# Kernel optimization log

Hardware: AMD Instinct MI355X
Metric: run time of the kernel (lower is better)

The kernel has to match this reference:

```python
import jax, jax.numpy as jnp
import numpy as np
import math
from jax import lax

B, T, C = 32, 512, 256
NL, NH, FF = 2, 4, 1024
DH = C // NH
NFREQ = 64   # n_even//2 for d_model=256 (even dims interleave sin/cos)
N_ODD = 128  # odd dims carry learned ramp a*t+b
MIN_P, MAX_P = 4.0, 10000.0


def setup_inputs() -> dict:
    key = jax.random.key(0)
    ks = jax.random.split(key, 16)
    def nrm(k, shape, s=0.02):
        return (jax.random.normal(k, shape) * s).astype(jnp.float32)
    x = jax.random.normal(ks[0], (B, T, C), jnp.float32)
    # strictly increasing normalized timestamps
    dts = jax.random.uniform(ks[1], (B, T), jnp.float32) * 0.02 + 1e-3
    ts = jnp.cumsum(dts, axis=1)
    return {
        "x": x, "ts": ts,
        "gru_Wih": nrm(ks[2], (3 * C, C)), "gru_Whh": nrm(ks[3], (3 * C, C)),
        "gru_bih": jnp.zeros((3 * C,), jnp.float32), "gru_bhh": jnp.zeros((3 * C,), jnp.float32),
        "ode_W": nrm(ks[4], (C, 4 * C)), "ode_b": jnp.zeros((C,), jnp.float32),
        "norm_ode_g": jnp.ones((C,), jnp.float32), "norm_ode_b": jnp.zeros((C,), jnp.float32),
        "norm_gru_g": jnp.ones((C,), jnp.float32), "norm_gru_b": jnp.zeros((C,), jnp.float32),
        "film_W": nrm(ks[5], (2 * C, C)), "film_b": jnp.zeros((2 * C,), jnp.float32),
        "te_a": nrm(ks[6], (N_ODD,), 1.0), "te_b": nrm(ks[7], (N_ODD,), 0.1),
        "qkv_W": nrm(ks[8], (NL, 3 * C, C)), "qkv_b": jnp.zeros((NL, 3 * C), jnp.float32),
        "out_W": nrm(ks[9], (NL, C, C)), "out_b": jnp.zeros((NL, C), jnp.float32),
        "ln1_g": jnp.ones((NL, C), jnp.float32), "ln1_b": jnp.zeros((NL, C), jnp.float32),
        "ln2_g": jnp.ones((NL, C), jnp.float32), "ln2_b": jnp.zeros((NL, C), jnp.float32),
        "ff1_W": nrm(ks[10], (NL, FF, C)), "ff1_b": jnp.zeros((NL, FF), jnp.float32),
        "ff2_W": nrm(ks[11], (NL, C, FF)), "ff2_b": jnp.zeros((NL, C), jnp.float32),
        "lnf_g": jnp.ones((C,), jnp.float32), "lnf_b": jnp.zeros((C,), jnp.float32),
    }


def _ln(x, g, b, eps=1e-5):
    m = x.mean(-1, keepdims=True)
    v = ((x - m) ** 2).mean(-1, keepdims=True)
    return (x - m) / jnp.sqrt(v + eps) * g + b


def _forward(x, ts, gru_Wih, gru_Whh, gru_bih, gru_bhh, ode_W, ode_b,
             norm_ode_g, norm_ode_b, norm_gru_g, norm_gru_b, film_W, film_b,
             te_a, te_b, qkv_W, qkv_b, out_W, out_b, ln1_g, ln1_b, ln2_g, ln2_b,
             ff1_W, ff1_b, ff2_W, ff2_b, lnf_g, lnf_b):
    Bx, Tx, Cx = x.shape

    def gru(xi, h):  # PyTorch GRUCell math
        gi = xi @ gru_Wih.T + gru_bih
        gh = h @ gru_Whh.T + gru_bhh
        ir, iz, inn = jnp.split(gi, 3, -1)
        hr, hz, hn = jnp.split(gh, 3, -1)
        r = jax.nn.sigmoid(ir + hr)
        z = jax.nn.sigmoid(iz + hz)
        n = jnp.tanh(inn + r * hn)
        return (1.0 - z) * n + z * h

    def step(h, inp):  # RK4 ODE jump + GRU jump per event
        xi, xp, dt = inp  # (B,C),(B,C),(B,1)
        dx = (xi - xp) / dt
        def f(hh):
            return jnp.tanh(jnp.concatenate([hh, xi, xp, dx], -1) @ ode_W.T + ode_b)
        k1 = f(h)
        k2 = f(h + 0.5 * dt * k1)
        k3 = f(h + 0.5 * dt * k2)
        k4 = f(h + dt * k3)
        h = h + dt / 6.0 * (k1 + 2.0 * k2 + 2.0 * k3 + k4)
        h = _ln(h, norm_ode_g, norm_ode_b)
        h = _ln(gru(xi, h), norm_gru_g, norm_gru_b)
        return h, h

    h0 = _ln(gru(x[:, 0], jnp.zeros((Bx, Cx), x.dtype)), norm_gru_g, norm_gru_b)
    xs = (x[:, 1:].swapaxes(0, 1), x[:, :-1].swapaxes(0, 1),
          (ts[:, 1:] - ts[:, :-1])[..., None].swapaxes(0, 1))
    _, ys = lax.scan(step, h0, xs)
    h = jnp.concatenate([h0[None], ys], 0).swapaxes(0, 1)  # (B,T,C)

    # FiLM params from hidden states
    gb = jax.nn.silu(h) @ film_W.T + film_b
    gamma, beta = jnp.split(gb, 2, -1)

    # TimeHybridEncoding: even dims interleaved sin/cos, odd dims learned ramp
    freqs = jnp.exp(-jnp.linspace(0.0, math.log(MAX_P / MIN_P), NFREQ)) * (2.0 * math.pi / MIN_P)
    phase = ts[..., None] * freqs  # (B,T,NFREQ)
    sc = jnp.stack([jnp.sin(phase), jnp.cos(phase)], -1).reshape(Bx, Tx, 2 * NFREQ)
    ramp = ts[..., None] * te_a + te_b  # (B,T,N_ODD)
    tme = jnp.zeros((Bx, Tx, Cx), x.dtype)
    tme = tme.at[..., 0::2].set(sc).at[..., 1::2].set(ramp)
    tme = (1.0 + gamma) * tme + beta

    # Pre-LN TransformerEncoder (eval mode: dropout off), relu FFN, final LN
    H = h + tme
    scale = 1.0 / jnp.sqrt(jnp.float32(DH))
    for l in range(NL):
        a = _ln(H, ln1_g[l], ln1_b[l])
        qkv = a @ qkv_W[l].T + qkv_b[l]
        q, k, v = jnp.split(qkv, 3, -1)
        q = q.reshape(Bx, Tx, NH, DH).transpose(0, 2, 1, 3)
        k = k.reshape(Bx, Tx, NH, DH).transpose(0, 2, 1, 3)
        v = v.reshape(Bx, Tx, NH, DH).transpose(0, 2, 1, 3)
        att = jax.nn.softmax(jnp.einsum('bhqd,bhkd->bhqk', q, k) * scale, axis=-1)
        o = jnp.einsum('bhqk,bhkd->bhqd', att, v).transpose(0, 2, 1, 3).reshape(Bx, Tx, Cx)
        H = H + o @ out_W[l].T + out_b[l]
        f2 = _ln(H, ln2_g[l], ln2_b[l])
        H = H + jax.nn.relu(f2 @ ff1_W[l].T + ff1_b[l]) @ ff2_W[l].T + ff2_b[l]
    return _ln(H, lnf_g, lnf_b)


def reference(x, ts, gru_Wih, gru_Whh, gru_bih, gru_bhh, ode_W, ode_b,
              norm_ode_g, norm_ode_b, norm_gru_g, norm_gru_b, film_W, film_b,
              te_a, te_b, qkv_W, qkv_b, out_W, out_b, ln1_g, ln1_b, ln2_g, ln2_b,
              ff1_W, ff1_b, ff2_W, ff2_b, lnf_g, lnf_b):
    return _forward(x, ts, gru_Wih, gru_Whh, gru_bih, gru_bhh, ode_W, ode_b,
                    norm_ode_g, norm_ode_b, norm_gru_g, norm_gru_b, film_W, film_b,
                    te_a, te_b, qkv_W, qkv_b, out_W, out_b, ln1_g, ln1_b, ln2_g, ln2_b,
                    ff1_W, ff1_b, ff2_W, ff2_b, lnf_g, lnf_b)
```

## Files before the change

### kernel.cpp

```cpp
#include <hip/hip_runtime.h>
#include <hip/hip_bf16.h>
#include <math.h>

typedef long long i64;

__device__ __forceinline__ float2 blockSum2_256(float a, float b, float* red) {
#pragma unroll
  for (int off = 32; off; off >>= 1) {
    a += __shfl_xor(a, off, 64);
    b += __shfl_xor(b, off, 64);
  }
  __syncthreads();
  if ((threadIdx.x & 63) == 0) {
    int w = threadIdx.x >> 6;
    red[w * 2 + 0] = a;
    red[w * 2 + 1] = b;
  }
  __syncthreads();
  return make_float2(red[0] + red[2] + red[4] + red[6],
                     red[1] + red[3] + red[5] + red[7]);
}

__device__ __forceinline__ float lnVal(float v, float g, float b, float* red) {
  float2 s = blockSum2_256(v, v * v, red);
  float mean = s.x * (1.0f / 256.0f);
  float var = s.y * (1.0f / 256.0f) - mean * mean;
  var = fmaxf(var, 0.0f);
  return (v - mean) * rsqrtf(var + 1e-5f) * g + b;
}

__device__ __forceinline__ double2 blockSum2d_1024(double a, double b, double* red) {
#pragma unroll
  for (int off = 32; off; off >>= 1) {
    a += __shfl_xor(a, off, 64);
    b += __shfl_xor(b, off, 64);
  }
  __syncthreads();
  if ((threadIdx.x & 63) == 0) {
    int w = threadIdx.x >> 6;
    red[w * 2 + 0] = a;
    red[w * 2 + 1] = b;
  }
  __syncthreads();
  double sa = 0.0, sb = 0.0;
#pragma unroll
  for (int i = 0; i < 16; ++i) { sa += red[i * 2]; sb += red[i * 2 + 1]; }
  double2 r; r.x = sa; r.y = sb; return r;
}

template <typename ACCT>
__global__ __launch_bounds__(256)
void gemm_nt_t(const float* __restrict__ A, int lda,
               const float* __restrict__ W, int ldw,
               const float* __restrict__ bias,
               const float* add,
               float* C, int ldc,
               int M, int N, int K, int relu)
{
  __shared__ float As[16][68];
  __shared__ float Ws[16][68];
  const int tid = threadIdx.x;
  const int tx = tid & 15, ty = tid >> 4;
  const int m0 = blockIdx.y * 64, n0 = blockIdx.x * 64;
  const int lrow = tid >> 2, lk = (tid & 3) << 2;
  ACCT acc[4][4] = {};
  for (int k0 = 0; k0 < K; k0 += 16) {
    float4 av = make_float4(0.f, 0.f, 0.f, 0.f);
    if (m0 + lrow < M) av = *(const float4*)(A + (i64)(m0 + lrow) * lda + k0 + lk);
    float4 wv = *(const float4*)(W + (i64)(n0 + lrow) * ldw + k0 + lk);
    As[lk + 0][lrow] = av.x; As[lk + 1][lrow] = av.y;
    As[lk + 2][lrow] = av.z; As[lk + 3][lrow] = av.w;
    Ws[lk + 0][lrow] = wv.x; Ws[lk + 1][lrow] = wv.y;
    Ws[lk + 2][lrow] = wv.z; Ws[lk + 3][lrow] = wv.w;
    __syncthreads();
#pragma unroll
    for (int kk = 0; kk < 16; ++kk) {
      ACCT a0 = (ACCT)As[kk][ty * 4 + 0], a1 = (ACCT)As[kk][ty * 4 + 1];
      ACCT a2 = (ACCT)As[kk][ty * 4 + 2], a3 = (ACCT)As[kk][ty * 4 + 3];
      ACCT b0 = (ACCT)Ws[kk][tx * 4 + 0], b1 = (ACCT)Ws[kk][tx * 4 + 1];
      ACCT b2 = (ACCT)Ws[kk][tx * 4 + 2], b3 = (ACCT)Ws[kk][tx * 4 + 3];
      acc[0][0] += a0 * b0; acc[0][1] += a0 * b1; acc[0][2] += a0 * b2; acc[0][3] += a0 * b3;
      acc[1][0] += a1 * b0; acc[1][1] += a1 * b1; acc[1][2] += a1 * b2; acc[1][3] += a1 * b3;
      acc[2][0] += a2 * b0; acc[2][1] += a2 * b1; acc[2][2] += a2 * b2; acc[2][3] += a2 * b3;
      acc[3][0] += a3 * b0; acc[3][1] += a3 * b1; acc[3][2] += a3 * b2; acc[3][3] += a3 * b3;
    }
    __syncthreads();
  }
#pragma unroll
  for (int i = 0; i < 4; ++i) {
    int m = m0 + ty * 4 + i;
    if (m >= M) continue;
#pragma unroll
    for (int j = 0; j < 4; ++j) {
      int n = n0 + tx * 4 + j;
      ACCT v = acc[i][j];
      if (bias) v += (ACCT)bias[n];
      if (relu) v = v > (ACCT)0 ? v : (ACCT)0;
      if (add) v += (ACCT)add[(i64)m * ldc + n];
      C[(i64)m * ldc + n] = (float)v;
    }
  }
}

__global__ __launch_bounds__(256)
void pack_weights(const float* __restrict__ odeW, const float* __restrict__ Whh,
                  float* __restrict__ W4h, float* __restrict__ W4hh)
{
  int idx = blockIdx.x * 256 + threadIdx.x;
  if (idx < 65536) {
    int j = idx >> 8, k = idx & 255;
    W4h[((k >> 2) << 10) + (j << 2) + (k & 3)] = odeW[j * 1024 + k];
  } else {
    int t = idx - 65536;
    int j3 = t >> 8, k = t & 255;
    W4hh[(k >> 2) * 3072 + (j3 << 2) + (k & 3)] = Whh[j3 * 256 + k];
  }
}

__global__ __launch_bounds__(256)
void dx_kernel(const float* __restrict__ x, const float* __restrict__ ts,
               float* __restrict__ dx)
{
  i64 row = blockIdx.x;
  int c = threadIdx.x;
  int t = (int)(row & 511);
  float v = 0.0f;
  if (t > 0) {
    double dt = (double)ts[row] - (double)ts[row - 1];
    v = (float)(((double)x[row * 256 + c] - (double)x[(row - 1) * 256 + c]) / dt);
  }
  dx[row * 256 + c] = v;
}

__global__ __launch_bounds__(256)
void silu_kernel(const float* __restrict__ in, float* __restrict__ out)
{
  i64 i = (i64)blockIdx.x * 256 + threadIdx.x;
  float v = in[i];
  out[i] = v / (1.0f + __expf(-v));
}

__global__ __launch_bounds__(256)
void fill_kernel(float* __restrict__ out, float v)
{
  i64 i = (i64)blockIdx.x * 256 + threadIdx.x;
  out[i] = v;
}

__device__ __forceinline__ float dot64f(const float4* __restrict__ w,
                                        const float* __restrict__ v)
{
  float a0 = 0.f, a1 = 0.f, a2 = 0.f, a3 = 0.f;
#pragma unroll
  for (int m = 0; m < 16; ++m) {
    float4 x = *(const float4*)(v + (m << 2));
    a0 = fmaf(w[m].x, x.x, a0);
    a1 = fmaf(w[m].y, x.y, a1);
    a2 = fmaf(w[m].z, x.z, a2);
    a3 = fmaf(w[m].w, x.w, a3);
  }
  return (a0 + a1) + (a2 + a3);
}

__global__ __launch_bounds__(1024, 4)
void scan_kernel(const float* __restrict__ gi, const float* __restrict__ u,
                 const float* __restrict__ ts,
                 const float* __restrict__ W4h, const float* __restrict__ W4hh,
                 const float* __restrict__ bhh,
                 const float* __restrict__ nog, const float* __restrict__ nob,
                 const float* __restrict__ ngg, const float* __restrict__ ngb,
                 float* __restrict__ hseq)
{
  const int b = blockIdx.x;
  const int t = threadIdx.x;
  const int j = t & 255;
  const int kq = t >> 8;
  const int kbase = kq << 6;

  __shared__ __align__(16) double hs[256];
  __shared__ __align__(16) float hsf[256];
  __shared__ __align__(16) float kb[256];
  __shared__ __align__(16) float predf[1024];
  __shared__ __align__(16) double predd[3][1024];
  __shared__ double red[32];

  float4 wreg[16];
#pragma unroll
  for (int m4 = 0; m4 < 16; ++m4)
    wreg[m4] = *(const float4*)(W4h + (((kq << 4) + m4) << 10) + (j << 2));
#pragma unroll
  for (int m4 = 0; m4 < 16; ++m4)
    asm volatile("" : "+v"(wreg[m4].x), "+v"(wreg[m4].y),
                      "+v"(wreg[m4].z), "+v"(wreg[m4].w));

  const double gng = (double)ngg[j], gnb = (double)ngb[j];
  const double gog = (double)nog[j], gob = (double)nob[j];
  const double bhr = (double)bhh[j], bhz = (double)bhh[256 + j], bhn = (double)bhh[512 + j];

  double h = 0.0;
  {
    const i64 row0 = (i64)b * 512;
    double h0 = 0.0;
    if (kq == 0) {
      double ir = (double)gi[row0 * 768 + j];
      double iz = (double)gi[row0 * 768 + 256 + j];
      double inn = (double)gi[row0 * 768 + 512 + j];
      double rr = 1.0 / (1.0 + exp(-(ir + bhr)));
      double zz = 1.0 / (1.0 + exp(-(iz + bhz)));
      double nn = tanh(inn + rr * bhn);
      h0 = (1.0 - zz) * nn;
    }
    double2 s0 = blockSum2d_1024(h0, h0 * h0, red);
    double mean = s0.x * (1.0 / 256.0);
    double var = s0.y * (1.0 / 256.0) - mean * mean;
    var = var > 0.0 ? var : 0.0;
    if (kq == 0) {
      h0 = (h0 - mean) / sqrt(var + 1e-5) * gng + gnb;
      hs[j] = h0; hsf[j] = (float)h0;
      hseq[row0 * 256 + j] = (float)h0;
      h = h0;
    }
    __syncthreads();
  }

  for (int s = 0; s < 511; ++s) {
    const double dt = (double)ts[b * 512 + s + 1] - (double)ts[b * 512 + s];
    const float dtf = (float)dt;
    const i64 row = (i64)(b * 512 + s + 1);

    float u_j = 0.f, ir2f = 0.f, iz2f = 0.f, in2f = 0.f;
    if (kq == 0) {
      u_j = u[row * 256 + j];
      ir2f = gi[row * 768 + j];
      iz2f = gi[row * 768 + 256 + j];
      in2f = gi[row * 768 + 512 + j];
    }

    float a_s = 0.f, k1s = 0.f, k2s = 0.f, k3s = 0.f, k4s = 0.f;
    predf[t] = dot64f(wreg, hsf + kbase);
    __syncthreads();
    if (kq == 0) {
      a_s = predf[j] + predf[j + 256] + predf[j + 512] + predf[j + 768] + u_j;
      k1s = tanhf(a_s);
      kb[j] = k1s;
    }
    __syncthreads();
    predf[t] = dot64f(wreg, kb + kbase);
    __syncthreads();
    if (kq == 0) {
      float bsum = predf[j] + predf[j + 256] + predf[j + 512] + predf[j + 768];
      k2s = tanhf(fmaf(0.5f * dtf, bsum, a_s));
      kb[j] = k2s;
    }
    __syncthreads();
    predf[t] = dot64f(wreg, kb + kbase);
    __syncthreads();
    if (kq == 0) {
      float bsum = predf[j] + predf[j + 256] + predf[j + 512] + predf[j + 768];
      k3s = tanhf(fmaf(0.5f * dtf, bsum, a_s));
      kb[j] = k3s;
    }
    __syncthreads();
    predf[t] = dot64f(wreg, kb + kbase);
    __syncthreads();
    if (kq == 0) {
      float bsum = predf[j] + predf[j + 256] + predf[j + 512] + predf[j + 768];
      k4s = tanhf(fmaf(dtf, bsum, a_s));
    }

    double hode = 0.0;
    if (kq == 0) {
      hode = h + dt * (1.0 / 6.0) *
             ((double)k1s + 2.0 * (double)k2s + 2.0 * (double)k3s + (double)k4s);
    }
    {
      double2 so = blockSum2d_1024(hode, hode * hode, red);
      double mean = so.x * (1.0 / 256.0);
      double var = so.y * (1.0 / 256.0) - mean * mean;
      var = var > 0.0 ? var : 0.0;
      if (kq == 0) {
        hode = (hode - mean) / sqrt(var + 1e-5) * gog + gob;
        hs[j] = hode;
      }
    }
    __syncthreads();

    {
      double g0 = 0.0, g1 = 0.0, g2 = 0.0;
#pragma unroll 2
      for (int m4 = 0; m4 < 16; ++m4) {
        const double2* hp = (const double2*)(hs + kbase + (m4 << 2));
        double2 ha = hp[0], hb = hp[1];
        const float* base = W4hh + ((kq << 4) + m4) * 3072 + (j << 2);
        float4 w0 = *(const float4*)(base);
        float4 w1 = *(const float4*)(base + 1024);
        float4 w2 = *(const float4*)(base + 2048);
        g0 += (double)w0.x * ha.x + (double)w0.y * ha.y + (double)w0.z * hb.x + (double)w0.w * hb.y;
        g1 += (double)w1.x * ha.x + (double)w1.y * ha.y + (double)w1.z * hb.x + (double)w1.w * hb.y;
        g2 += (double)w2.x * ha.x + (double)w2.y * ha.y + (double)w2.z * hb.x + (double)w2.w * hb.y;
      }
      predd[0][t] = g0; predd[1][t] = g1; predd[2][t] = g2;
    }
    __syncthreads();

    double hg = 0.0;
    if (kq == 0) {
      double g0 = predd[0][j] + predd[0][j + 256] + predd[0][j + 512] + predd[0][j + 768];
      double g1 = predd[1][j] + predd[1][j + 256] + predd[1][j + 512] + predd[1][j + 768];
      double g2 = predd[2][j] + predd[2][j + 256] + predd[2][j + 512] + predd[2][j + 768];
      double hodev = hs[j];
      double rr = 1.0 / (1.0 + exp(-((double)ir2f + g0 + bhr)));
      double zz = 1.0 / (1.0 + exp(-((double)iz2f + g1 + bhz)));
      double nn = tanh((double)in2f + rr * (g2 + bhn));
      hg = (1.0 - zz) * nn + zz * hodev;
    }
    {
      double2 sg = blockSum2d_1024(hg, hg * hg, red);
      double mean = sg.x * (1.0 / 256.0);
      double var = sg.y * (1.0 / 256.0) - mean * mean;
      var = var > 0.0 ? var : 0.0;
      if (kq == 0) {
        hg = (hg - mean) / sqrt(var + 1e-5) * gng + gnb;
        hs[j] = hg; hsf[j] = (float)hg;
        hseq[row * 256 + j] = (float)hg;
        h = hg;
      }
    }
    __syncthreads();
  }
}

__global__ __launch_bounds__(256)
void tme_kernel(const float* __restrict__ hseq, const float* __restrict__ gb,
                const float* __restrict__ ts,
                const float* __restrict__ te_a, const float* __restrict__ te_b,
                float* __restrict__ H)
{
  i64 idx = (i64)blockIdx.x * 256 + threadIdx.x;
  int c = (int)(idx & 255);
  i64 bt = idx >> 8;
  double tv = (double)ts[bt];
  double tme;
  if (c & 1) {
    int i = c >> 1;
    tme = tv * (double)te_a[i] + (double)te_b[i];
  } else {
    int f = c >> 2;
    double freq = exp(-(log(2500.0) / 63.0) * (double)f) * 1.5707963267948966;
    double ph = tv * freq;
    tme = ((c >> 1) & 1) ? cos(ph) : sin(ph);
  }
  float gamma = gb[bt * 512 + c];
  float beta = gb[bt * 512 + 256 + c];
  H[idx] = hseq[idx] + (1.0f + gamma) * (float)tme + beta;
}

__global__ __launch_bounds__(256)
void ln256_f32(const float* __restrict__ in, const float* __restrict__ g,
               const float* __restrict__ b, float* __restrict__ out)
{
  __shared__ float red[8];
  i64 row = blockIdx.x;
  float v = in[row * 256 + threadIdx.x];
  out[row * 256 + threadIdx.x] = lnVal(v, g[threadIdx.x], b[threadIdx.x], red);
}

__global__ __launch_bounds__(256)
void attn_kernel(const float* __restrict__ qkv, float* __restrict__ O)
{
  __shared__ float Qs[32][68];
  __shared__ float Ks[64][68];
  __shared__ float Vs[64][68];
  int bid = blockIdx.x;
  int qb = bid & 15, bh = bid >> 4;
  int h = bh & 3, b = bh >> 2;
  int tid = threadIdx.x;
  int r = tid >> 3, dg = tid & 7;
  int lane = tid & 63;
  int q0 = qb * 32;
  i64 base = (i64)b * 512 * 768;
  {
    int rr = tid >> 3, c8 = (tid & 7) * 8;
    const float* src = qkv + base + (i64)(q0 + rr) * 768 + h * 64 + c8;
    *(float4*)&Qs[rr][c8] = *(const float4*)src;
    *(float4*)&Qs[rr][c8 + 4] = *(const float4*)(src + 4);
  }
  float m = -1e30f, l = 0.0f;
  float o[8] = {0.f, 0.f, 0.f, 0.f, 0.f, 0.f, 0.f, 0.f};
  for (int kt = 0; kt < 8; ++kt) {
    __syncthreads();
    {
      int kr = tid >> 2, c16 = (tid & 3) * 16;
      const float* srcK = qkv + base + (i64)(kt * 64 + kr) * 768 + 256 + h * 64 + c16;
      const float* srcV = srcK + 256;
#pragma unroll
      for (int ii = 0; ii < 4; ++ii) {
        *(float4*)&Ks[kr][c16 + ii * 4] = *(const float4*)(srcK + ii * 4);
        *(float4*)&Vs[kr][c16 + ii * 4] = *(const float4*)(srcV + ii * 4);
      }
    }
    __syncthreads();
    float s[8] = {0.f, 0.f, 0.f, 0.f, 0.f, 0.f, 0.f, 0.f};
#pragma unroll
    for (int d4 = 0; d4 < 16; ++d4) {
      float4 qv = *(const float4*)&Qs[r][d4 * 4];
#pragma unroll
      for (int i = 0; i < 8; ++i) {
        float4 kv = *(const float4*)&Ks[dg * 8 + i][d4 * 4];
        s[i] += qv.x * kv.x + qv.y * kv.y + qv.z * kv.z + qv.w * kv.w;
      }
    }
    float ms = -1e30f;
#pragma unroll
    for (int i = 0; i < 8; ++i) { s[i] *= 0.125f; ms = fmaxf(ms, s[i]); }
    ms = fmaxf(ms, __shfl_xor(ms, 1, 64));
    ms = fmaxf(ms, __shfl_xor(ms, 2, 64));
    ms = fmaxf(ms, __shfl_xor(ms, 4, 64));
    float mnew = fmaxf(m, ms);
    float p[8];
    float ls = 0.0f;
#pragma unroll
    for (int i = 0; i < 8; ++i) { p[i] = __expf(s[i] - mnew); ls += p[i]; }
    ls += __shfl_xor(ls, 1, 64);
    ls += __shfl_xor(ls, 2, 64);
    ls += __shfl_xor(ls, 4, 64);
    float alpha = __expf(m - mnew);
    l = l * alpha + ls;
#pragma unroll
    for (int i = 0; i < 8; ++i) o[i] *= alpha;
    m = mnew;
#pragma unroll
    for (int i = 0; i < 8; ++i) {
#pragma unroll
      for (int dgk = 0; dgk < 8; ++dgk) {
        float pv = __shfl(p[i], (lane & 56) | dgk, 64);
        int kk = dgk * 8 + i;
        float4 v0 = *(const float4*)&Vs[kk][dg * 8];
        float4 v1 = *(const float4*)&Vs[kk][dg * 8 + 4];
        o[0] += pv * v0.x; o[1] += pv * v0.y; o[2] += pv * v0.z; o[3] += pv * v0.w;
        o[4] += pv * v1.x; o[5] += pv * v1.y; o[6] += pv * v1.z; o[7] += pv * v1.w;
      }
    }
  }
  float invl = 1.0f / l;
  float* dst = O + (i64)(b * 512 + q0 + r) * 256 + h * 64 + dg * 8;
  float4 r0 = make_float4(o[0] * invl, o[1] * invl, o[2] * invl, o[3] * invl);
  float4 r1 = make_float4(o[4] * invl, o[5] * invl, o[6] * invl, o[7] * invl);
  *(float4*)dst = r0;
  *(float4*)(dst + 4) = r1;
}

extern "C" void kernel_launch(void* const* d_in, const int* in_sizes, int n_in,
                              void* d_out, int out_size, void* d_ws, size_t ws_size,
                              hipStream_t stream)
{
  (void)in_sizes; (void)n_in; (void)out_size;
  const float* x       = (const float*)d_in[0];
  const float* ts      = (const float*)d_in[1];
  const float* gru_Wih = (const float*)d_in[2];
  const float* gru_Whh = (const float*)d_in[3];
  const float* gru_bih = (const float*)d_in[4];
  const float* gru_bhh = (const float*)d_in[5];
  const float* ode_W   = (const float*)d_in[6];
  const float* ode_b   = (const float*)d_in[7];
  const float* nog     = (const float*)d_in[8];
  const float* nob     = (const float*)d_in[9];
  const float* ngg     = (const float*)d_in[10];
  const float* ngb     = (const float*)d_in[11];
  const float* film_W  = (const float*)d_in[12];
  const float* film_b  = (const float*)d_in[13];
  const float* te_a    = (const float*)d_in[14];
  const float* te_bb   = (const float*)d_in[15];
  const float* qkv_W   = (const float*)d_in[16];
  const float* qkv_b   = (const float*)d_in[17];
  const float* out_W   = (const float*)d_in[18];
  const float* out_b   = (const float*)d_in[19];
  const float* ln1_g   = (const float*)d_in[20];
  const float* ln1_b   = (const float*)d_in[21];
  const float* ln2_g   = (const float*)d_in[22];
  const float* ln2_b   = (const float*)d_in[23];
  const float* ff1_W   = (const float*)d_in[24];
  const float* ff1_b   = (const float*)d_in[25];
  const float* ff2_W   = (const float*)d_in[26];
  const float* ff2_b   = (const float*)d_in[27];
  const float* lnf_g   = (const float*)d_in[28];
  const float* lnf_b   = (const float*)d_in[29];

  const size_t NEED = 25427968ull * 4ull;
  if (ws_size < NEED) {
    fill_kernel<<<16384, 256, 0, stream>>>((float*)d_out, 1000.0f);
    return;
  }
  float* ws   = (float*)d_ws;
  float* W4h  = ws;
  float* W4hh = ws + 65536;
  float* SA   = ws + 262144;
  float* SB   = ws + 4456448;
  float* Hb   = ws + 8650752;
  float* BIG  = ws + 12845056;

  float* u = SA;  float* sh = SA;   float* aln = SA;  float* f2 = SA;
  float* dxb = SB; float* hseq = SB; float* Obuf = SB; float* ff1o = SB;
  float* gi = BIG; float* gb = BIG;  float* qkvb = BIG;

  const int MROW = 32 * 512;

  pack_weights<<<1024, 256, 0, stream>>>(ode_W, gru_Whh, W4h, W4hh);
  dx_kernel<<<MROW, 256, 0, stream>>>(x, ts, dxb);
  gemm_nt_t<double><<<dim3(12, 256), 256, 0, stream>>>(x, 256, gru_Wih, 256, gru_bih,
                                                       nullptr, gi, 768, MROW, 768, 256, 0);
  gemm_nt_t<double><<<dim3(4, 256), 256, 0, stream>>>(x + 256, 256, ode_W + 256, 1024, ode_b,
                                                      nullptr, u + 256, 256, MROW - 1, 256, 256, 0);
  gemm_nt_t<double><<<dim3(4, 256), 256, 0, stream>>>(x, 256, ode_W + 512, 1024, nullptr,
                                                      u + 256, u + 256, 256, MROW - 1, 256, 256, 0);
  gemm_nt_t<double><<<dim3(4, 256), 256, 0, stream>>>(dxb + 256, 256, ode_W + 768, 1024, nullptr,
                                                      u + 256, u + 256, 256, MROW - 1, 256, 256, 0);
  scan_kernel<<<32, 1024, 0, stream>>>(gi, u, ts, W4h, W4hh, gru_bhh,
                                       nog, nob, ngg, ngb, hseq);
  silu_kernel<<<MROW, 256, 0, stream>>>(hseq, sh);
  gemm_nt_t<float><<<dim3(8, 256), 256, 0, stream>>>(sh, 256, film_W, 256, film_b, nullptr,
                                                     gb, 512, MROW, 512, 256, 0);
  tme_kernel<<<MROW, 256, 0, stream>>>(hseq, gb, ts, te_a, te_bb, Hb);

  for (int l = 0; l < 2; ++l) {
    ln256_f32<<<MROW, 256, 0, stream>>>(Hb, ln1_g + 256 * l, ln1_b + 256 * l, aln);
    gemm_nt_t<float><<<dim3(12, 256), 256, 0, stream>>>(aln, 256, qkv_W + (i64)196608 * l, 256,
                                                        qkv_b + 768 * l, nullptr,
                                                        qkvb, 768, MROW, 768, 256, 0);
    attn_kernel<<<2048, 256, 0, stream>>>(qkvb, Obuf);
    gemm_nt_t<float><<<dim3(4, 256), 256, 0, stream>>>(Obuf, 256, out_W + (i64)65536 * l, 256,
                                                       out_b + 256 * l, Hb, Hb, 256,
                                                       MROW, 256, 256, 0);
    ln256_f32<<<MROW, 256, 0, stream>>>(Hb, ln2_g + 256 * l, ln2_b + 256 * l, f2);
    for (int c = 0; c < 4; ++c) {
      const int r0 = c * 4096;
      gemm_nt_t<float><<<dim3(16, 64), 256, 0, stream>>>(f2 + (i64)r0 * 256, 256,
                                                         ff1_W + (i64)262144 * l, 256,
                                                         ff1_b + 1024 * l, nullptr,
                                                         ff1o, 1024, 4096, 1024, 256, 1);
      gemm_nt_t<float><<<dim3(4, 64), 256, 0, stream>>>(ff1o, 1024,
                                                        ff2_W + (i64)262144 * l, 1024,
                                                        ff2_b + 256 * l,
                                                        Hb + (i64)r0 * 256, Hb + (i64)r0 * 256, 256,
                                                        4096, 256, 1024, 0);
    }
  }
  ln256_f32<<<MROW, 256, 0, stream>>>(Hb, lnf_g, lnf_b, (float*)d_out);
}
```

Before: 10.20 ms.

## Stage ODE weights as bf16 in LDS for RK4 stages, drop register-resident weights

The scan kernel no longer keeps the fp32 ODE weight tile in 64 VGPRs per thread. It packs the weights to bf16 in 128KB of dynamic LDS and uses them for RK4 stages 2-4. Stage 1 reads fp32 weights from global memory each step, and the three double-precision GRU partial-sum buffers are merged into one scratch buffer reused with extra barriers. This lowers register pressure, which may let the compiler schedule better or avoid spills. In exchange it adds LDS traffic, more syncthreads per step and reduced precision in the ODE stage sums.

Measured after the change: 12.58 ms. 23.3% more time.

```diff
diff --git a/kernel.cpp b/kernel.cpp
--- a/kernel.cpp
+++ b/kernel.cpp
@@ -147,17 +147,23 @@
   out[i] = v;
 }
 
-__device__ __forceinline__ float dot64f(const float4* __restrict__ w,
-                                        const float* __restrict__ v)
+__device__ __forceinline__ unsigned short f2bf(float x) {
+  __hip_bfloat16 b = __float2bfloat16(x);
+  return *reinterpret_cast<unsigned short*>(&b);
+}
+
+__device__ __forceinline__ float dot64bf(const uint2* __restrict__ wbrow, int j,
+                                         const float* __restrict__ v)
 {
   float a0 = 0.f, a1 = 0.f, a2 = 0.f, a3 = 0.f;
 #pragma unroll
   for (int m = 0; m < 16; ++m) {
-    float4 x = *(const float4*)(v + (m << 2));
-    a0 = fmaf(w[m].x, x.x, a0);
-    a1 = fmaf(w[m].y, x.y, a1);
-    a2 = fmaf(w[m].z, x.z, a2);
-    a3 = fmaf(w[m].w, x.w, a3);
+    uint2 w = wbrow[(m << 8) + j];
+    float4 kv = *(const float4*)(v + (m << 2));
+    a0 = fmaf(__uint_as_float(w.x << 16), kv.x, a0);
+    a1 = fmaf(__uint_as_float(w.x & 0xffff0000u), kv.y, a1);
+    a2 = fmaf(__uint_as_float(w.y << 16), kv.z, a2);
+    a3 = fmaf(__uint_as_float(w.y & 0xffff0000u), kv.w, a3);
   }
   return (a0 + a1) + (a2 + a3);
 }
@@ -171,27 +177,28 @@
                  const float* __restrict__ ngg, const float* __restrict__ ngb,
                  float* __restrict__ hseq)
 {
+  extern __shared__ __align__(16) char smem[];
+  uint2*  wb   = (uint2*)smem;
+  double* hs   = (double*)(smem + 131072);
+  float*  hsf  = (float*)(smem + 133120);
+  float*  kb   = (float*)(smem + 134144);
+  double* sc_d = (double*)(smem + 135168);
+  float*  sc_f = (float*)(smem + 135168);
+  double* red  = (double*)(smem + 143360);
+
   const int b = blockIdx.x;
   const int t = threadIdx.x;
   const int j = t & 255;
   const int kq = t >> 8;
   const int kbase = kq << 6;
-
-  __shared__ __align__(16) double hs[256];
-  __shared__ __align__(16) float hsf[256];
-  __shared__ __align__(16) float kb[256];
-  __shared__ __align__(16) float predf[1024];
-  __shared__ __align__(16) double predd[3][1024];
-  __shared__ double red[32];
-
-  float4 wreg[16];
-#pragma unroll
-  for (int m4 = 0; m4 < 16; ++m4)
-    wreg[m4] = *(const float4*)(W4h + (((kq << 4) + m4) << 10) + (j << 2));
-#pragma unroll
-  for (int m4 = 0; m4 < 16; ++m4)
-    asm volatile("" : "+v"(wreg[m4].x), "+v"(wreg[m4].y),
-                      "+v"(wreg[m4].z), "+v"(wreg[m4].w));
+  const uint2* wbrow = wb + (kq << 12);
+
+  for (int e = t; e < 16384; e += 1024) {
+    int row = e >> 8, j2 = e & 255;
+    float4 w4 = *(const float4*)(W4h + (row << 10) + (j2 << 2));
+    wb[e] = make_uint2((unsigned)f2bf(w4.x) | ((unsigned)f2bf(w4.y) << 16),
+                       (unsigned)f2bf(w4.z) | ((unsigned)f2bf(w4.w) << 16));
+  }
 
   const double gng = (double)ngg[j], gnb = (double)ngb[j];
   const double gog = (double)nog[j], gob = (double)nob[j];
@@ -237,34 +244,44 @@
     }
 
     float a_s = 0.f, k1s = 0.f, k2s = 0.f, k3s = 0.f, k4s = 0.f;
-    predf[t] = dot64f(wreg, hsf + kbase);
-    __syncthreads();
-    if (kq == 0) {
-      a_s = predf[j] + predf[j + 256] + predf[j + 512] + predf[j + 768] + u_j;
+    {
+      float a0 = 0.f, a1 = 0.f, a2 = 0.f, a3 = 0.f;
+#pragma unroll
+      for (int m4 = 0; m4 < 16; ++m4) {
+        float4 w = *(const float4*)(W4h + (((kq << 4) + m4) << 10) + (j << 2));
+        float4 hv = *(const float4*)(hsf + kbase + (m4 << 2));
+        a0 = fmaf(w.x, hv.x, a0); a1 = fmaf(w.y, hv.y, a1);
+        a2 = fmaf(w.z, hv.z, a2); a3 = fmaf(w.w, hv.w, a3);
+      }
+      sc_f[t] = (a0 + a1) + (a2 + a3);
+    }
+    __syncthreads();
+    if (kq == 0) {
+      a_s = sc_f[j] + sc_f[j + 256] + sc_f[j + 512] + sc_f[j + 768] + u_j;
       k1s = tanhf(a_s);
       kb[j] = k1s;
     }
     __syncthreads();
-    predf[t] = dot64f(wreg, kb + kbase);
-    __syncthreads();
-    if (kq == 0) {
-      float bsum = predf[j] + predf[j + 256] + predf[j + 512] + predf[j + 768];
+    sc_f[t] = dot64bf(wbrow, j, kb + kbase);
+    __syncthreads();
+    if (kq == 0) {
+      float bsum = sc_f[j] + sc_f[j + 256] + sc_f[j + 512] + sc_f[j + 768];
       k2s = tanhf(fmaf(0.5f * dtf, bsum, a_s));
       kb[j] = k2s;
     }
     __syncthreads();
-    predf[t] = dot64f(wreg, kb + kbase);
-    __syncthreads();
-    if (kq == 0) {
-      float bsum = predf[j] + predf[j + 256] + predf[j + 512] + predf[j + 768];
+    sc_f[t] = dot64bf(wbrow, j, kb + kbase);
+    __syncthreads();
+    if (kq == 0) {
+      float bsum = sc_f[j] + sc_f[j + 256] + sc_f[j + 512] + sc_f[j + 768];
       k3s = tanhf(fmaf(0.5f * dtf, bsum, a_s));
       kb[j] = k3s;
     }
     __syncthreads();
-    predf[t] = dot64f(wreg, kb + kbase);
-    __syncthreads();
-    if (kq == 0) {
-      float bsum = predf[j] + predf[j + 256] + predf[j + 512] + predf[j + 768];
+    sc_f[t] = dot64bf(wbrow, j, kb + kbase);
+    __syncthreads();
+    if (kq == 0) {
+      float bsum = sc_f[j] + sc_f[j + 256] + sc_f[j + 512] + sc_f[j + 768];
       k4s = tanhf(fmaf(dtf, bsum, a_s));
     }
 
@@ -285,8 +302,8 @@
     }
     __syncthreads();
 
+    double g0 = 0.0, g1 = 0.0, g2 = 0.0;
     {
-      double g0 = 0.0, g1 = 0.0, g2 = 0.0;
 #pragma unroll 2
       for (int m4 = 0; m4 < 16; ++m4) {
         const double2* hp = (const double2*)(hs + kbase + (m4 << 2));
@@ -299,19 +316,22 @@
         g1 += (double)w1.x * ha.x + (double)w1.y * ha.y + (double)w1.z * hb.x + (double)w1.w * hb.y;
         g2 += (double)w2.x * ha.x + (double)w2.y * ha.y + (double)w2.z * hb.x + (double)w2.w * hb.y;
       }
-      predd[0][t] = g0; predd[1][t] = g1; predd[2][t] = g2;
-    }
-    __syncthreads();
-
+    }
+    double G0 = 0.0, G1 = 0.0, G2 = 0.0;
+    sc_d[t] = g0; __syncthreads();
+    if (kq == 0) G0 = sc_d[j] + sc_d[j + 256] + sc_d[j + 512] + sc_d[j + 768];
+    __syncthreads();
+    sc_d[t] = g1; __syncthreads();
+    if (kq == 0) G1 = sc_d[j] + sc_d[j + 256] + sc_d[j + 512] + sc_d[j + 768];
+    __syncthreads();
+    sc_d[t] = g2; __syncthreads();
     double hg = 0.0;
     if (kq == 0) {
-      double g0 = predd[0][j] + predd[0][j + 256] + predd[0][j + 512] + predd[0][j + 768];
-      double g1 = predd[1][j] + predd[1][j + 256] + predd[1][j + 512] + predd[1][j + 768];
-      double g2 = predd[2][j] + predd[2][j + 256] + predd[2][j + 512] + predd[2][j + 768];
+      G2 = sc_d[j] + sc_d[j + 256] + sc_d[j + 512] + sc_d[j + 768];
       double hodev = hs[j];
-      double rr = 1.0 / (1.0 + exp(-((double)ir2f + g0 + bhr)));
-      double zz = 1.0 / (1.0 + exp(-((double)iz2f + g1 + bhz)));
-      double nn = tanh((double)in2f + rr * (g2 + bhn));
+      double rr = 1.0 / (1.0 + exp(-((double)ir2f + G0 + bhr)));
+      double zz = 1.0 / (1.0 + exp(-((double)iz2f + G1 + bhz)));
+      double nn = tanh((double)in2f + rr * (G2 + bhn));
       hg = (1.0 - zz) * nn + zz * hodev;
     }
     {
@@ -504,6 +524,14 @@
   float* gi = BIG; float* gb = BIG;  float* qkvb = BIG;
 
   const int MROW = 32 * 512;
+  const int SCAN_LDS = 143616;
+
+  static int lds_attr_set = 0;
+  if (!lds_attr_set) {
+    (void)hipFuncSetAttribute((const void*)scan_kernel,
+                              hipFuncAttributeMaxDynamicSharedMemorySize, SCAN_LDS);
+    lds_attr_set = 1;
+  }
 
   pack_weights<<<1024, 256, 0, stream>>>(ode_W, gru_Whh, W4h, W4hh);
   dx_kernel<<<MROW, 256, 0, stream>>>(x, ts, dxb);
@@ -515,8 +543,8 @@
                                                       u + 256, u + 256, 256, MROW - 1, 256, 256, 0);
   gemm_nt_t<double><<<dim3(4, 256), 256, 0, stream>>>(dxb + 256, 256, ode_W + 768, 1024, nullptr,
                                                       u + 256, u + 256, 256, MROW - 1, 256, 256, 0);
-  scan_kernel<<<32, 1024, 0, stream>>>(gi, u, ts, W4h, W4hh, gru_bhh,
-                                       nog, nob, ngg, ngb, hseq);
+  scan_kernel<<<32, 1024, SCAN_LDS, stream>>>(gi, u, ts, W4h, W4hh, gru_bhh,
+                                              nog, nob, ngg, ngb, hseq);
   silu_kernel<<<MROW, 256, 0, stream>>>(hseq, sh);
   gemm_nt_t<float><<<dim3(8, 256), 256, 0, stream>>>(sh, 256, film_W, 256, film_b, nullptr,
                                                      gb, 512, MROW, 512, 256, 0);
```

## Fold LayerNorm into scan matvecs via precomputed weight row sums

Applied to the files above, without the earlier changes.

Rewrites the serial GRU/ODE scan so each LayerNorm is applied algebraically after the matvec. The matvec runs on the raw state scaled by gamma, then the result is corrected with mean/invstd and precomputed row sums of W·gamma and W·beta, produced by a new pack_rowsums kernel. This lets the matvecs start before the block reduction for the norm statistics finishes, removing several barriers per step. The ODE weights are no longer held in registers and are re-read from global memory each step, and the change introduces cancellation risk in the mean-correction term.

After: 9.426 ms. 7.6% less time.

```diff
diff --git a/kernel.cpp b/kernel.cpp
--- a/kernel.cpp
+++ b/kernel.cpp
@@ -29,23 +29,12 @@
   return (v - mean) * rsqrtf(var + 1e-5f) * g + b;
 }
 
-__device__ __forceinline__ double2 blockSum2d_1024(double a, double b, double* red) {
+__device__ __forceinline__ void waveRed2d(double& a, double& b) {
 #pragma unroll
   for (int off = 32; off; off >>= 1) {
     a += __shfl_xor(a, off, 64);
     b += __shfl_xor(b, off, 64);
   }
-  __syncthreads();
-  if ((threadIdx.x & 63) == 0) {
-    int w = threadIdx.x >> 6;
-    red[w * 2 + 0] = a;
-    red[w * 2 + 1] = b;
-  }
-  __syncthreads();
-  double sa = 0.0, sb = 0.0;
-#pragma unroll
-  for (int i = 0; i < 16; ++i) { sa += red[i * 2]; sb += red[i * 2 + 1]; }
-  double2 r; r.x = sa; r.y = sb; return r;
 }
 
 template <typename ACCT>
@@ -118,6 +107,33 @@
 }
 
 __global__ __launch_bounds__(256)
+void pack_rowsums(const float* __restrict__ odeW, const float* __restrict__ Whh,
+                  const float* __restrict__ ngg, const float* __restrict__ ngb,
+                  const float* __restrict__ nog, const float* __restrict__ nob,
+                  double* __restrict__ Sd)
+{
+  int r = blockIdx.x * 256 + threadIdx.x;
+  if (r < 256) {
+    double s1 = 0.0, s0 = 0.0;
+    for (int k = 0; k < 256; ++k) {
+      double w = (double)odeW[r * 1024 + k];
+      s1 += w * (double)ngg[k];
+      s0 += w * (double)ngb[k];
+    }
+    Sd[r] = s1; Sd[256 + r] = s0;
+  } else {
+    int j3 = r - 256;
+    double s1 = 0.0, s0 = 0.0;
+    for (int k = 0; k < 256; ++k) {
+      double w = (double)Whh[j3 * 256 + k];
+      s1 += w * (double)nog[k];
+      s0 += w * (double)nob[k];
+    }
+    Sd[512 + j3] = s1; Sd[1280 + j3] = s0;
+  }
+}
+
+__global__ __launch_bounds__(256)
 void dx_kernel(const float* __restrict__ x, const float* __restrict__ ts,
                float* __restrict__ dx)
 {
@@ -147,17 +163,16 @@
   out[i] = v;
 }
 
-__device__ __forceinline__ float dot64f(const float4* __restrict__ w,
+__device__ __forceinline__ float dot64s(const float* __restrict__ W, int kq, int j,
                                         const float* __restrict__ v)
 {
   float a0 = 0.f, a1 = 0.f, a2 = 0.f, a3 = 0.f;
 #pragma unroll
-  for (int m = 0; m < 16; ++m) {
-    float4 x = *(const float4*)(v + (m << 2));
-    a0 = fmaf(w[m].x, x.x, a0);
-    a1 = fmaf(w[m].y, x.y, a1);
-    a2 = fmaf(w[m].z, x.z, a2);
-    a3 = fmaf(w[m].w, x.w, a3);
+  for (int m4 = 0; m4 < 16; ++m4) {
+    float4 w = *(const float4*)(W + (((kq << 4) + m4) << 10) + (j << 2));
+    float4 x = *(const float4*)(v + (m4 << 2));
+    a0 = fmaf(w.x, x.x, a0); a1 = fmaf(w.y, x.y, a1);
+    a2 = fmaf(w.z, x.z, a2); a3 = fmaf(w.w, x.w, a3);
   }
   return (a0 + a1) + (a2 + a3);
 }
@@ -166,6 +181,7 @@
 void scan_kernel(const float* __restrict__ gi, const float* __restrict__ u,
                  const float* __restrict__ ts,
                  const float* __restrict__ W4h, const float* __restrict__ W4hh,
+                 const double* __restrict__ Sd,
                  const float* __restrict__ bhh,
                  const float* __restrict__ nog, const float* __restrict__ nob,
                  const float* __restrict__ ngg, const float* __restrict__ ngb,
@@ -176,31 +192,29 @@
   const int j = t & 255;
   const int kq = t >> 8;
   const int kbase = kq << 6;
-
-  __shared__ __align__(16) double hs[256];
-  __shared__ __align__(16) float hsf[256];
-  __shared__ __align__(16) float kb[256];
-  __shared__ __align__(16) float predf[1024];
+  const int lane = t & 63;
+  const int wv = t >> 6;
+
+  __shared__ __align__(16) float  hraw2f[256];
+  __shared__ __align__(16) double vr2[256];
+  __shared__ __align__(16) float  kb[256];
+  __shared__ __align__(16) float  sc_f[1024];
   __shared__ __align__(16) double predd[3][1024];
-  __shared__ double red[32];
-
-  float4 wreg[16];
-#pragma unroll
-  for (int m4 = 0; m4 < 16; ++m4)
-    wreg[m4] = *(const float4*)(W4h + (((kq << 4) + m4) << 10) + (j << 2));
-#pragma unroll
-  for (int m4 = 0; m4 < 16; ++m4)
-    asm volatile("" : "+v"(wreg[m4].x), "+v"(wreg[m4].y),
-                      "+v"(wreg[m4].z), "+v"(wreg[m4].w));
+  __shared__ double redv[8];
+  __shared__ double redh[8];
 
   const double gng = (double)ngg[j], gnb = (double)ngb[j];
   const double gog = (double)nog[j], gob = (double)nob[j];
   const double bhr = (double)bhh[j], bhz = (double)bhh[256 + j], bhn = (double)bhh[512 + j];
-
-  double h = 0.0;
+  const double sa1 = Sd[j], sa0 = Sd[256 + j];
+  const double sg1r = Sd[512 + j],  sg0r = Sd[1280 + j];
+  const double sg1z = Sd[768 + j],  sg0z = Sd[1536 + j];
+  const double sg1n = Sd[1024 + j], sg0n = Sd[1792 + j];
+
+  double hLN = 0.0, hg_raw = 0.0, mg = 0.0, invg = 1.0;
+
   {
     const i64 row0 = (i64)b * 512;
-    double h0 = 0.0;
     if (kq == 0) {
       double ir = (double)gi[row0 * 768 + j];
       double iz = (double)gi[row0 * 768 + 256 + j];
@@ -208,20 +222,25 @@
       double rr = 1.0 / (1.0 + exp(-(ir + bhr)));
       double zz = 1.0 / (1.0 + exp(-(iz + bhz)));
       double nn = tanh(inn + rr * bhn);
-      h0 = (1.0 - zz) * nn;
-    }
-    double2 s0 = blockSum2d_1024(h0, h0 * h0, red);
-    double mean = s0.x * (1.0 / 256.0);
-    double var = s0.y * (1.0 / 256.0) - mean * mean;
-    var = var > 0.0 ? var : 0.0;
-    if (kq == 0) {
-      h0 = (h0 - mean) / sqrt(var + 1e-5) * gng + gnb;
-      hs[j] = h0; hsf[j] = (float)h0;
-      hseq[row0 * 256 + j] = (float)h0;
-      h = h0;
-    }
-    __syncthreads();
-  }
+      hg_raw = (1.0 - zz) * nn;
+      hraw2f[j] = (float)(gng * hg_raw);
+      double sa = hg_raw, sb = hg_raw * hg_raw;
+      waveRed2d(sa, sb);
+      if (lane == 0) { redh[wv * 2] = sa; redh[wv * 2 + 1] = sb; }
+    }
+    __syncthreads();
+    if (kq == 0) {
+      double S = redh[0] + redh[2] + redh[4] + redh[6];
+      double Q = redh[1] + redh[3] + redh[5] + redh[7];
+      mg = S * (1.0 / 256.0);
+      double var = Q * (1.0 / 256.0) - mg * mg;
+      var = var > 0.0 ? var : 0.0;
+      invg = 1.0 / sqrt(var + 1e-5);
+      hLN = (hg_raw - mg) * invg * gng + gnb;
+      hseq[row0 * 256 + j] = (float)hLN;
+    }
+  }
+  __syncthreads();
 
   for (int s = 0; s < 511; ++s) {
     const double dt = (double)ts[b * 512 + s + 1] - (double)ts[b * 512 + s];
@@ -236,97 +255,96 @@
       in2f = gi[row * 768 + 512 + j];
     }
 
+    sc_f[t] = dot64s(W4h, kq, j, hraw2f + kbase);
+    __syncthreads();
     float a_s = 0.f, k1s = 0.f, k2s = 0.f, k3s = 0.f, k4s = 0.f;
-    predf[t] = dot64f(wreg, hsf + kbase);
-    __syncthreads();
-    if (kq == 0) {
-      a_s = predf[j] + predf[j + 256] + predf[j + 512] + predf[j + 768] + u_j;
+    if (kq == 0) {
+      double psum = (double)(sc_f[j] + sc_f[j + 256] + sc_f[j + 512] + sc_f[j + 768]);
+      double a_d = psum * invg - mg * invg * sa1 + sa0 + (double)u_j;
+      a_s = (float)a_d;
       k1s = tanhf(a_s);
       kb[j] = k1s;
     }
     __syncthreads();
-    predf[t] = dot64f(wreg, kb + kbase);
-    __syncthreads();
-    if (kq == 0) {
-      float bsum = predf[j] + predf[j + 256] + predf[j + 512] + predf[j + 768];
-      k2s = tanhf(fmaf(0.5f * dtf, bsum, a_s));
+    sc_f[t] = dot64s(W4h, kq, j, kb + kbase);
+    __syncthreads();
+    if (kq == 0) {
+      float bs = sc_f[j] + sc_f[j + 256] + sc_f[j + 512] + sc_f[j + 768];
+      k2s = tanhf(fmaf(0.5f * dtf, bs, a_s));
       kb[j] = k2s;
     }
     __syncthreads();
-    predf[t] = dot64f(wreg, kb + kbase);
-    __syncthreads();
-    if (kq == 0) {
-      float bsum = predf[j] + predf[j + 256] + predf[j + 512] + predf[j + 768];
-      k3s = tanhf(fmaf(0.5f * dtf, bsum, a_s));
+    sc_f[t] = dot64s(W4h, kq, j, kb + kbase);
+    __syncthreads();
+    if (kq == 0) {
+      float bs = sc_f[j] + sc_f[j + 256] + sc_f[j + 512] + sc_f[j + 768];
+      k3s = tanhf(fmaf(0.5f * dtf, bs, a_s));
       kb[j] = k3s;
     }
     __syncthreads();
-    predf[t] = dot64f(wreg, kb + kbase);
-    __syncthreads();
-    if (kq == 0) {
-      float bsum = predf[j] + predf[j + 256] + predf[j + 512] + predf[j + 768];
-      k4s = tanhf(fmaf(dtf, bsum, a_s));
-    }
-
-    double hode = 0.0;
-    if (kq == 0) {
-      hode = h + dt * (1.0 / 6.0) *
-             ((double)k1s + 2.0 * (double)k2s + 2.0 * (double)k3s + (double)k4s);
-    }
-    {
-      double2 so = blockSum2d_1024(hode, hode * hode, red);
-      double mean = so.x * (1.0 / 256.0);
-      double var = so.y * (1.0 / 256.0) - mean * mean;
-      var = var > 0.0 ? var : 0.0;
-      if (kq == 0) {
-        hode = (hode - mean) / sqrt(var + 1e-5) * gog + gob;
-        hs[j] = hode;
-      }
-    }
-    __syncthreads();
-
+    sc_f[t] = dot64s(W4h, kq, j, kb + kbase);
+    __syncthreads();
+    double hode_raw = 0.0;
+    if (kq == 0) {
+      float bs = sc_f[j] + sc_f[j + 256] + sc_f[j + 512] + sc_f[j + 768];
+      k4s = tanhf(fmaf(dtf, bs, a_s));
+      hode_raw = hLN + dt * (1.0 / 6.0) *
+                 ((double)k1s + 2.0 * (double)k2s + 2.0 * (double)k3s + (double)k4s);
+      vr2[j] = gog * hode_raw;
+      double sa = hode_raw, sb = hode_raw * hode_raw;
+      waveRed2d(sa, sb);
+      if (lane == 0) { redv[wv * 2] = sa; redv[wv * 2 + 1] = sb; }
+    }
+    __syncthreads();
     {
       double g0 = 0.0, g1 = 0.0, g2 = 0.0;
 #pragma unroll 2
       for (int m4 = 0; m4 < 16; ++m4) {
-        const double2* hp = (const double2*)(hs + kbase + (m4 << 2));
-        double2 ha = hp[0], hb = hp[1];
+        const double2* hp = (const double2*)(vr2 + kbase + (m4 << 2));
+        double2 ha = hp[0], hb2 = hp[1];
         const float* base = W4hh + ((kq << 4) + m4) * 3072 + (j << 2);
         float4 w0 = *(const float4*)(base);
         float4 w1 = *(const float4*)(base + 1024);
         float4 w2 = *(const float4*)(base + 2048);
-        g0 += (double)w0.x * ha.x + (double)w0.y * ha.y + (double)w0.z * hb.x + (double)w0.w * hb.y;
-        g1 += (double)w1.x * ha.x + (double)w1.y * ha.y + (double)w1.z * hb.x + (double)w1.w * hb.y;
-        g2 += (double)w2.x * ha.x + (double)w2.y * ha.y + (double)w2.z * hb.x + (double)w2.w * hb.y;
+        g0 += (double)w0.x * ha.x + (double)w0.y * ha.y + (double)w0.z * hb2.x + (double)w0.w * hb2.y;
+        g1 += (double)w1.x * ha.x + (double)w1.y * ha.y + (double)w1.z * hb2.x + (double)w1.w * hb2.y;
+        g2 += (double)w2.x * ha.x + (double)w2.y * ha.y + (double)w2.z * hb2.x + (double)w2.w * hb2.y;
       }
       predd[0][t] = g0; predd[1][t] = g1; predd[2][t] = g2;
     }
     __syncthreads();
-
-    double hg = 0.0;
-    if (kq == 0) {
-      double g0 = predd[0][j] + predd[0][j + 256] + predd[0][j + 512] + predd[0][j + 768];
-      double g1 = predd[1][j] + predd[1][j + 256] + predd[1][j + 512] + predd[1][j + 768];
-      double g2 = predd[2][j] + predd[2][j + 256] + predd[2][j + 512] + predd[2][j + 768];
-      double hodev = hs[j];
-      double rr = 1.0 / (1.0 + exp(-((double)ir2f + g0 + bhr)));
-      double zz = 1.0 / (1.0 + exp(-((double)iz2f + g1 + bhz)));
-      double nn = tanh((double)in2f + rr * (g2 + bhn));
-      hg = (1.0 - zz) * nn + zz * hodev;
-    }
-    {
-      double2 sg = blockSum2d_1024(hg, hg * hg, red);
-      double mean = sg.x * (1.0 / 256.0);
-      double var = sg.y * (1.0 / 256.0) - mean * mean;
+    if (kq == 0) {
+      double mo = (redv[0] + redv[2] + redv[4] + redv[6]) * (1.0 / 256.0);
+      double qo = (redv[1] + redv[3] + redv[5] + redv[7]) * (1.0 / 256.0);
+      double var = qo - mo * mo; var = var > 0.0 ? var : 0.0;
+      double invo = 1.0 / sqrt(var + 1e-5);
+      double G0 = (predd[0][j] + predd[0][j + 256] + predd[0][j + 512] + predd[0][j + 768]) * invo
+                  - mo * invo * sg1r + sg0r;
+      double G1 = (predd[1][j] + predd[1][j + 256] + predd[1][j + 512] + predd[1][j + 768]) * invo
+                  - mo * invo * sg1z + sg0z;
+      double G2 = (predd[2][j] + predd[2][j + 256] + predd[2][j + 512] + predd[2][j + 768]) * invo
+                  - mo * invo * sg1n + sg0n;
+      double rr = 1.0 / (1.0 + exp(-((double)ir2f + G0 + bhr)));
+      double zz = 1.0 / (1.0 + exp(-((double)iz2f + G1 + bhz)));
+      double nn = tanh((double)in2f + rr * (G2 + bhn));
+      double hodeLN = (hode_raw - mo) * invo * gog + gob;
+      hg_raw = (1.0 - zz) * nn + zz * hodeLN;
+      hraw2f[j] = (float)(gng * hg_raw);
+      double sa = hg_raw, sb = hg_raw * hg_raw;
+      waveRed2d(sa, sb);
+      if (lane == 0) { redh[wv * 2] = sa; redh[wv * 2 + 1] = sb; }
+    }
+    __syncthreads();
+    if (kq == 0) {
+      double S = redh[0] + redh[2] + redh[4] + redh[6];
+      double Q = redh[1] + redh[3] + redh[5] + redh[7];
+      mg = S * (1.0 / 256.0);
+      double var = Q * (1.0 / 256.0) - mg * mg;
       var = var > 0.0 ? var : 0.0;
-      if (kq == 0) {
-        hg = (hg - mean) / sqrt(var + 1e-5) * gng + gnb;
-        hs[j] = hg; hsf[j] = (float)hg;
-        hseq[row * 256 + j] = (float)hg;
-        h = hg;
-      }
-    }
-    __syncthreads();
+      invg = 1.0 / sqrt(var + 1e-5);
+      hLN = (hg_raw - mg) * invg * gng + gnb;
+      hseq[row * 256 + j] = (float)hLN;
+    }
   }
 }
 
@@ -486,18 +504,19 @@
   const float* lnf_g   = (const float*)d_in[28];
   const float* lnf_b   = (const float*)d_in[29];
 
-  const size_t NEED = 25427968ull * 4ull;
+  const size_t NEED = 25432064ull * 4ull;
   if (ws_size < NEED) {
     fill_kernel<<<16384, 256, 0, stream>>>((float*)d_out, 1000.0f);
     return;
   }
-  float* ws   = (float*)d_ws;
-  float* W4h  = ws;
-  float* W4hh = ws + 65536;
-  float* SA   = ws + 262144;
-  float* SB   = ws + 4456448;
-  float* Hb   = ws + 8650752;
-  float* BIG  = ws + 12845056;
+  float*  ws   = (float*)d_ws;
+  float*  W4h  = ws;
+  float*  W4hh = ws + 65536;
+  double* Sd   = (double*)(ws + 262144);
+  float*  SA   = ws + 266240;
+  float*  SB   = ws + 4460544;
+  float*  Hb   = ws + 8654848;
+  float*  BIG  = ws + 12849152;
 
   float* u = SA;  float* sh = SA;   float* aln = SA;  float* f2 = SA;
   float* dxb = SB; float* hseq = SB; float* Obuf = SB; float* ff1o = SB;
@@ -506,6 +525,7 @@
   const int MROW = 32 * 512;
 
   pack_weights<<<1024, 256, 0, stream>>>(ode_W, gru_Whh, W4h, W4hh);
+  pack_rowsums<<<4, 256, 0, stream>>>(ode_W, gru_Whh, ngg, ngb, nog, nob, Sd);
   dx_kernel<<<MROW, 256, 0, stream>>>(x, ts, dxb);
   gemm_nt_t<double><<<dim3(12, 256), 256, 0, stream>>>(x, 256, gru_Wih, 256, gru_bih,
                                                        nullptr, gi, 768, MROW, 768, 256, 0);
@@ -515,7 +535,7 @@
                                                       u + 256, u + 256, 256, MROW - 1, 256, 256, 0);
   gemm_nt_t<double><<<dim3(4, 256), 256, 0, stream>>>(dxb + 256, 256, ode_W + 768, 1024, nullptr,
                                                       u + 256, u + 256, 256, MROW - 1, 256, 256, 0);
-  scan_kernel<<<32, 1024, 0, stream>>>(gi, u, ts, W4h, W4hh, gru_bhh,
+  scan_kernel<<<32, 1024, 0, stream>>>(gi, u, ts, W4h, W4hh, Sd, gru_bhh,
                                        nog, nob, ngg, ngb, hseq);
   silu_kernel<<<MROW, 256, 0, stream>>>(hseq, sh);
   gemm_nt_t<float><<<dim3(8, 256), 256, 0, stream>>>(sh, 256, film_W, 256, film_b, nullptr,
```
